# Kernel tuning notes

Hardware: AMD Instinct MI355X
Metric: run time of the kernel (lower is better)

Reference implementation:

```python
import jax, jax.numpy as jnp
import numpy as np

B, S, D, H = 2, 2048, 1024, 16
W = D // H  # head width = 64


def setup_inputs() -> dict:
    key = jax.random.key(0)
    ks = jax.random.split(key, 10)
    std = 1.0 / np.sqrt(D)
    return {
        "x": jax.random.normal(ks[0], (B, S, D), jnp.float32),
        "seg": jax.random.randint(ks[1], (B, S), 0, 2, jnp.int64),
        "Wq": jax.random.normal(ks[2], (D, D), jnp.float32) * std,
        "bq": jnp.zeros((D,), jnp.float32),
        "Wk": jax.random.normal(ks[3], (D, D), jnp.float32) * std,
        "bk": jnp.zeros((D,), jnp.float32),
        "Wv": jax.random.normal(ks[4], (D, D), jnp.float32) * std,
        "bv": jnp.zeros((D,), jnp.float32),
        "Wo": jax.random.normal(ks[5], (D, D), jnp.float32) * std,
        "bo": jnp.zeros((D,), jnp.float32),
    }


def reference(x, seg, Wq, bq, Wk, bk, Wv, bv, Wo, bo):
    # QKV projections: (B,S,D)
    q = x @ Wq + bq
    k = x @ Wk + bk
    v = x @ Wv + bv
    # split heads -> (B,H,S,W)
    def heads(t):
        return t.reshape(B, S, H, W).transpose(0, 2, 1, 3)
    q, k, v = heads(q), heads(k), heads(v)
    scale = 1.0 / np.sqrt(W).astype(np.float32)
    scores = jnp.einsum("bhqw,bhkw->bhqk", q, k) * scale  # (B,H,S,S)
    # causal mask: strictly-upper-triangular entries -> -inf
    causal = jnp.tril(jnp.ones((S, S), dtype=bool))
    scores = jnp.where(causal, scores, -jnp.inf)
    attn = jax.nn.softmax(scores, axis=-1)
    h = jnp.einsum("bhqk,bhkw->bhqw", attn, v)  # (B,H,S,W)
    h = h.transpose(0, 2, 1, 3).reshape(B, S, D)  # merge heads
    return h @ Wo + bo
```

## Files before the change

### kernel.cpp

```cpp
#include <hip/hip_runtime.h>

#define BB 2
#define SS 2048
#define DD 1024
#define HH 16
#define WW 64
#define MM (BB*SS)

typedef float f32x4 __attribute__((ext_vector_type(4)));
typedef short s16x8 __attribute__((ext_vector_type(8)));
typedef short s16x4 __attribute__((ext_vector_type(4)));

__device__ __forceinline__ unsigned short f2bf(float f) {
  return __builtin_bit_cast(unsigned short, (__bf16)f);
}
__device__ __forceinline__ float bf2f(unsigned short u) {
  return (float)__builtin_bit_cast(__bf16, u);
}
__device__ __forceinline__ void dma16(const unsigned short* g, unsigned short* l) {
  __builtin_amdgcn_global_load_lds(
      (const __attribute__((address_space(1))) unsigned int*)g,
      (__attribute__((address_space(3))) unsigned int*)l, 16, 0, 0);
}

__global__ __launch_bounds__(256) void k_prep(const float* __restrict__ x,
                                              unsigned short* __restrict__ xb,
                                              const float* __restrict__ W0,
                                              const float* __restrict__ W1,
                                              const float* __restrict__ W2,
                                              const float* __restrict__ W3,
                                              unsigned short* __restrict__ T0,
                                              unsigned short* __restrict__ T1,
                                              unsigned short* __restrict__ T2,
                                              unsigned short* __restrict__ T3) {
  if (blockIdx.z >= 4) {
    int blk = (blockIdx.z - 4) * 1024 + blockIdx.y * 32 + blockIdx.x;
    int i = (blk * 256 + threadIdx.x) * 4;
    float4 v = *(const float4*)(x + i);
    *(ushort4*)(xb + i) = make_ushort4(f2bf(v.x), f2bf(v.y), f2bf(v.z), f2bf(v.w));
    return;
  }
  const float* Wm = blockIdx.z == 0 ? W0 : blockIdx.z == 1 ? W1 : blockIdx.z == 2 ? W2 : W3;
  unsigned short* Wt = blockIdx.z == 0 ? T0 : blockIdx.z == 1 ? T1 : blockIdx.z == 2 ? T2 : T3;
  __shared__ float tile[32][33];
  int bn = blockIdx.x * 32;
  int bk = blockIdx.y * 32;
  int tx = threadIdx.x & 31;
  int ty = threadIdx.x >> 5;
#pragma unroll
  for (int r = 0; r < 4; ++r)
    tile[ty + r * 8][tx] = Wm[(bk + ty + r * 8) * DD + bn + tx];
  __syncthreads();
#pragma unroll
  for (int r = 0; r < 4; ++r)
    Wt[(bn + ty + r * 8) * DD + bk + tx] = f2bf(tile[tx][ty + r * 8]);
}

__global__ __launch_bounds__(256, 3) void k_gemm_qkv(const unsigned short* __restrict__ A,
                                                     const unsigned short* __restrict__ Wcat,
                                                     const float* __restrict__ bq,
                                                     const float* __restrict__ bk,
                                                     const float* __restrict__ bv,
                                                     unsigned short* __restrict__ Qo,
                                                     unsigned short* __restrict__ Ko,
                                                     unsigned short* __restrict__ Vo) {
  __shared__ __align__(16) unsigned short As[2][128 * 32];
  __shared__ __align__(16) unsigned short Bs[2][128 * 32];
  const int widx = blockIdx.x >> 3;
  const int n0 = (blockIdx.x & 7) * 128;
  const int m0 = blockIdx.y * 128;
  const unsigned short* Bt = Wcat + (size_t)widx * DD * DD;
  const float* bias = widx == 0 ? bq : widx == 1 ? bk : bv;
  unsigned short* outp = widx == 0 ? Qo : widx == 1 ? Ko : Vo;
  const float oscale = widx == 0 ? 0.125f * 1.4426950408889634f : 1.0f;
  const int t = threadIdx.x;
  const int wv = t >> 6, lane = t & 63;
  const int quad = lane >> 4, l16 = lane & 15;
  const int wm = (wv >> 1) * 64, wn = (wv & 1) * 64;
  const unsigned short* srcA[2];
  const unsigned short* srcB[2];
  int dstoff[2];
#pragma unroll
  for (int d = 0; d < 2; ++d) {
    int s = d * 256 + wv * 64 + lane;
    int r = s >> 2, pb = s & 3;
    int lc = ((pb ^ (r & 3)) << 3);
    srcA[d] = A + (size_t)(m0 + r) * DD + lc;
    srcB[d] = Bt + (size_t)(n0 + r) * DD + lc;
    dstoff[d] = (d * 256 + wv * 64) * 8;
  }
  f32x4 acc[4][4] = {};

#pragma unroll
  for (int d = 0; d < 2; ++d) {
    dma16(srcA[d], &As[0][dstoff[d]]);
    dma16(srcB[d], &Bs[0][dstoff[d]]);
  }

  for (int it = 0; it < DD / 32; ++it) {
    asm volatile("s_waitcnt vmcnt(0)" ::: "memory");
    __syncthreads();
    if (it + 1 < DD / 32) {
      const int nb = (it + 1) & 1;
      const int k1 = (it + 1) * 32;
#pragma unroll
      for (int d = 0; d < 2; ++d) {
        dma16(srcA[d] + k1, &As[nb][dstoff[d]]);
        dma16(srcB[d] + k1, &Bs[nb][dstoff[d]]);
      }
    }
    const unsigned short* Asb = As[it & 1];
    const unsigned short* Bsb = Bs[it & 1];
    s16x8 af[4], bfr[4];
#pragma unroll
    for (int mi = 0; mi < 4; ++mi) {
      int ra = wm + mi * 16 + l16;
      af[mi] = *(const s16x8*)(Asb + ra * 32 + ((quad ^ (ra & 3)) << 3));
    }
#pragma unroll
    for (int ni = 0; ni < 4; ++ni) {
      int rb = wn + ni * 16 + l16;
      bfr[ni] = *(const s16x8*)(Bsb + rb * 32 + ((quad ^ (rb & 3)) << 3));
    }
#pragma unroll
    for (int mi = 0; mi < 4; ++mi)
#pragma unroll
      for (int ni = 0; ni < 4; ++ni)
        acc[mi][ni] = __builtin_amdgcn_mfma_f32_16x16x32_bf16(af[mi], bfr[ni], acc[mi][ni], 0, 0, 0);
  }

#pragma unroll
  for (int mi = 0; mi < 4; ++mi) {
#pragma unroll
    for (int ni = 0; ni < 4; ++ni) {
      int col = n0 + wn + ni * 16 + l16;
      float bb = bias[col];
      int h = col >> 6, w = col & 63;
#pragma unroll
      for (int r = 0; r < 4; ++r) {
        int row = m0 + wm + mi * 16 + quad * 4 + r;
        float v = (acc[mi][ni][r] + bb) * oscale;
        int b = row >> 11, s = row & (SS - 1);
        long off;
        if (widx == 2) off = (long)(b * HH + h) * (SS * WW) + (long)w * SS + s;
        else           off = (long)(b * HH + h) * (SS * WW) + (long)s * WW + w;
        outp[off] = f2bf(v);
      }
    }
  }
}

__global__ __launch_bounds__(256, 3) void k_gemm_out(const unsigned short* __restrict__ A,
                                                     const unsigned short* __restrict__ Bt,
                                                     const float* __restrict__ bias,
                                                     float* __restrict__ out_f) {
  __shared__ __align__(16) unsigned short As[2][128 * 32];
  __shared__ __align__(16) unsigned short Bs[2][64 * 32];
  const int m0 = blockIdx.y * 128, n0 = blockIdx.x * 64;
  const int t = threadIdx.x;
  const int wv = t >> 6, lane = t & 63;
  const int quad = lane >> 4, l16 = lane & 15;
  const int wm = (wv >> 1) * 64, wn = (wv & 1) * 32;
  const unsigned short* srcA[2];
  int dstA[2];
#pragma unroll
  for (int d = 0; d < 2; ++d) {
    int s = d * 256 + wv * 64 + lane;
    int r = s >> 2, pb = s & 3;
    int lc = ((pb ^ (r & 3)) << 3);
    srcA[d] = A + (size_t)(m0 + r) * DD + lc;
    dstA[d] = (d * 256 + wv * 64) * 8;
  }
  const int sB = wv * 64 + lane;
  const int rB = sB >> 2, pbB = sB & 3;
  const unsigned short* srcB = Bt + (size_t)(n0 + rB) * DD + ((pbB ^ (rB & 3)) << 3);
  const int dstB = (wv * 64) * 8;
  f32x4 acc[4][2] = {};

#pragma unroll
  for (int d = 0; d < 2; ++d) dma16(srcA[d], &As[0][dstA[d]]);
  dma16(srcB, &Bs[0][dstB]);

  for (int it = 0; it < DD / 32; ++it) {
    asm volatile("s_waitcnt vmcnt(0)" ::: "memory");
    __syncthreads();
    if (it + 1 < DD / 32) {
      const int nb = (it + 1) & 1;
      const int k1 = (it + 1) * 32;
#pragma unroll
      for (int d = 0; d < 2; ++d) dma16(srcA[d] + k1, &As[nb][dstA[d]]);
      dma16(srcB + k1, &Bs[nb][dstB]);
    }
    const unsigned short* Asb = As[it & 1];
    const unsigned short* Bsb = Bs[it & 1];
    s16x8 af[4], bfr[2];
#pragma unroll
    for (int mi = 0; mi < 4; ++mi) {
      int ra = wm + mi * 16 + l16;
      af[mi] = *(const s16x8*)(Asb + ra * 32 + ((quad ^ (ra & 3)) << 3));
    }
#pragma unroll
    for (int ni = 0; ni < 2; ++ni) {
      int rb = wn + ni * 16 + l16;
      bfr[ni] = *(const s16x8*)(Bsb + rb * 32 + ((quad ^ (rb & 3)) << 3));
    }
#pragma unroll
    for (int mi = 0; mi < 4; ++mi)
#pragma unroll
      for (int ni = 0; ni < 2; ++ni)
        acc[mi][ni] = __builtin_amdgcn_mfma_f32_16x16x32_bf16(af[mi], bfr[ni], acc[mi][ni], 0, 0, 0);
  }

#pragma unroll
  for (int mi = 0; mi < 4; ++mi)
#pragma unroll
    for (int ni = 0; ni < 2; ++ni) {
      int col = n0 + wn + ni * 16 + l16;
      float bb = bias[col];
#pragma unroll
      for (int r = 0; r < 4; ++r) {
        int row = m0 + wm + mi * 16 + quad * 4 + r;
        out_f[row * DD + col] = acc[mi][ni][r] + bb;
      }
    }
}

__global__ __launch_bounds__(256, 2) void k_attn_mfma(const unsigned short* __restrict__ Q,
                                                      const unsigned short* __restrict__ K,
                                                      const unsigned short* __restrict__ Vt,
                                                      unsigned short* __restrict__ hm) {
  __shared__ __align__(16) unsigned short Kbuf[2][128 * 64];
  __shared__ __align__(16) unsigned short Vbuf[2][64 * 128];
  const int id = blockIdx.y * 16 + blockIdx.x;
  const int xcd = id & 7;
  const int j = id >> 3;
  const int bh = xcd * 4 + (j & 3);
  const int px = j >> 2;
  const int pairp = px >> 1;
  const int qh = px & 1;
  const int t = threadIdx.x;
  const int wv = t >> 6, lane = t & 63;
  const int quad = lane >> 4, l16 = lane & 15;
  const unsigned short* Qp = Q + (size_t)bh * SS * WW;
  const unsigned short* Kp = K + (size_t)bh * SS * WW;
  const unsigned short* Vp = Vt + (size_t)bh * WW * SS;
  const int b = bh >> 4, h = bh & 15;

  const int rrK = lane >> 3;
  const int kswz = (((lane & 7) ^ rrK) << 3);

  for (int sp = 0; sp < 2; ++sp) {
    const int strip = sp == 0 ? pairp : 15 - pairp;
    const int qs = strip * 128;
    const int qb = qs + qh * 64 + wv * 16;

    s16x8 qf[2];
#pragma unroll
    for (int c = 0; c < 2; ++c)
      qf[c] = *(const s16x8*)(Qp + (qb + l16) * WW + c * 32 + quad * 8);

    f32x4 O[4] = {};
    float l = 0.f;

    const int nkt = strip + 1;

#pragma unroll
    for (int d = 0; d < 4; ++d) {
      const int D = wv * 4 + d;
      dma16(Kp + (size_t)(D * 8 + rrK) * WW + kswz, &Kbuf[0][D * 512]);
      const int vrow = D * 4 + quad;
      dma16(Vp + (size_t)vrow * SS + (((lane & 15) ^ (vrow & 7)) << 3), &Vbuf[0][D * 512]);
    }

    for (int kt = 0; kt < nkt; ++kt) {
      const int kb = kt * 128;
      asm volatile("s_waitcnt vmcnt(0)" ::: "memory");
      __syncthreads();
      if (kt + 1 < nkt) {
        const int nb = (kt + 1) & 1;
        const int kbn = kb + 128;
#pragma unroll
        for (int d = 0; d < 4; ++d) {
          const int D = wv * 4 + d;
          dma16(Kp + (size_t)(kbn + D * 8 + rrK) * WW + kswz, &Kbuf[nb][D * 512]);
          const int vrow = D * 4 + quad;
          dma16(Vp + (size_t)vrow * SS + kbn + (((lane & 15) ^ (vrow & 7)) << 3),
                &Vbuf[nb][D * 512]);
        }
      }
      const unsigned short* Kb_ = Kbuf[kt & 1];
      const unsigned short* Vb_ = Vbuf[kt & 1];

      s16x8 kf[8][2];
#pragma unroll
      for (int mt = 0; mt < 8; ++mt)
#pragma unroll
        for (int c = 0; c < 2; ++c)
          kf[mt][c] = *(const s16x8*)(Kb_ + (mt * 16 + l16) * 64 + (((c * 4 + quad) ^ (l16 & 7)) << 3));

      f32x4 sc[8] = {};
      __builtin_amdgcn_s_setprio(1);
#pragma unroll
      for (int mt = 0; mt < 8; ++mt)
#pragma unroll
        for (int c = 0; c < 2; ++c)
          sc[mt] = __builtin_amdgcn_mfma_f32_16x16x32_bf16(kf[mt][c], qf[c], sc[mt], 0, 0, 0);
      __builtin_amdgcn_s_setprio(0);

      if (kt == nkt - 1) {
#pragma unroll
        for (int mt = 0; mt < 8; ++mt)
#pragma unroll
          for (int r = 0; r < 4; ++r)
            if (kb + mt * 16 + quad * 4 + r > qb + l16)
              sc[mt][r] = -__builtin_inff();
      }

#pragma unroll
      for (int mt = 0; mt < 8; ++mt)
#pragma unroll
        for (int r = 0; r < 4; ++r)
          sc[mt][r] = __builtin_amdgcn_exp2f(sc[mt][r]);

      s16x8 pf[4];
#pragma unroll
      for (int c = 0; c < 4; ++c) {
#pragma unroll
        for (int e = 0; e < 4; ++e) {
          pf[c][e]     = (short)f2bf(sc[2 * c][e]);
          pf[c][4 + e] = (short)f2bf(sc[2 * c + 1][e]);
        }
      }

      float ts[8];
#pragma unroll
      for (int mt = 0; mt < 8; ++mt)
        ts[mt] = (sc[mt][0] + sc[mt][1]) + (sc[mt][2] + sc[mt][3]);
      l += ((ts[0] + ts[1]) + (ts[2] + ts[3])) + ((ts[4] + ts[5]) + (ts[6] + ts[7]));

      const int xr = l16 & 7;
      __builtin_amdgcn_s_setprio(1);
#pragma unroll
      for (int ni = 0; ni < 4; ++ni) {
        const unsigned short* vrp = Vb_ + (ni * 16 + l16) * 128 + ((quad & 1) << 2);
#pragma unroll
        for (int c = 0; c < 4; ++c) {
          const int blo = (4 * c + (quad >> 1)) ^ xr;
          const int bhi = (4 * c + 2 + (quad >> 1)) ^ xr;
          s16x4 vlo = *(const s16x4*)(vrp + (blo << 3));
          s16x4 vhi = *(const s16x4*)(vrp + (bhi << 3));
          s16x8 vfc = __builtin_shufflevector(vlo, vhi, 0, 1, 2, 3, 4, 5, 6, 7);
          O[ni] = __builtin_amdgcn_mfma_f32_16x16x32_bf16(pf[c], vfc, O[ni], 0, 0, 0);
        }
      }
      __builtin_amdgcn_s_setprio(0);
    }

    l += __shfl_xor(l, 16);
    l += __shfl_xor(l, 32);
#pragma unroll
    for (int r = 0; r < 4; ++r) {
      const float linv = 1.f / __shfl(l, quad * 4 + r);
      const int q = qb + quad * 4 + r;
#pragma unroll
      for (int ni = 0; ni < 4; ++ni)
        hm[(size_t)(b * SS + q) * DD + h * WW + ni * 16 + l16] = f2bf(O[ni][r] * linv);
    }
    __syncthreads();
  }
}

extern "C" void kernel_launch(void* const* d_in, const int* in_sizes, int n_in,
                              void* d_out, int out_size, void* d_ws, size_t ws_size,
                              hipStream_t stream) {
  const float* x  = (const float*)d_in[0];
  const float* Wq = (const float*)d_in[2];
  const float* bq = (const float*)d_in[3];
  const float* Wk = (const float*)d_in[4];
  const float* bk = (const float*)d_in[5];
  const float* Wv = (const float*)d_in[6];
  const float* bv = (const float*)d_in[7];
  const float* Wo = (const float*)d_in[8];
  const float* bo = (const float*)d_in[9];
  float* out = (float*)d_out;

  char* ws = (char*)d_ws;
  unsigned short* xb   = (unsigned short*)(ws);
  unsigned short* Wcat = (unsigned short*)(ws + (size_t)( 8 << 20));
  unsigned short* Wtq  = Wcat;
  unsigned short* Wtk  = Wcat + (size_t)DD * DD;
  unsigned short* Wtv  = Wcat + (size_t)2 * DD * DD;
  unsigned short* Wto  = (unsigned short*)(ws + (size_t)(14 << 20));
  unsigned short* Qb   = (unsigned short*)(ws + (size_t)(16 << 20));
  unsigned short* Kb   = (unsigned short*)(ws + (size_t)(24 << 20));
  unsigned short* Vtb  = (unsigned short*)(ws + (size_t)(32 << 20));
  unsigned short* hm   = (unsigned short*)(ws + (size_t)(40 << 20));

  dim3 pg(32, 32, 8);
  k_prep<<<pg, 256, 0, stream>>>(x, xb, Wq, Wk, Wv, Wo, Wtq, Wtk, Wtv, Wto);

  dim3 gq(24, MM / 128);
  k_gemm_qkv<<<gq, 256, 0, stream>>>(xb, Wcat, bq, bk, bv, Qb, Kb, Vtb);

  dim3 ag(16, BB * HH);
  k_attn_mfma<<<ag, 256, 0, stream>>>(Qb, Kb, Vtb, hm);

  dim3 go(DD / 64, MM / 128);
  k_gemm_out<<<go, 256, 0, stream>>>(hm, Wto, bo, out);
}
```

Before: 188.3 us.

## Fuse all four stages into one persistent kernel with grid-wide barriers

Merges the prep/transposition, QKV GEMM, attention and output GEMM kernels into a single persistent 512-block kernel that loops over virtual block indices and separates stages with a software grid barrier built on global atomics. The goal is to remove three kernel launch gaps and their tail drains. In exchange every stage runs with a fixed 512-block grid at 2 blocks per CU, the QKV GEMM loses its previous 3-block occupancy hint, and correctness depends on all 512 blocks being co-resident. The barrier counter and generation live in device globals that persist across calls.

```diff
diff --git a/kernel.cpp b/kernel.cpp
--- a/kernel.cpp
+++ b/kernel.cpp
@@ -14,359 +14,373 @@
 __device__ __forceinline__ unsigned short f2bf(float f) {
   return __builtin_bit_cast(unsigned short, (__bf16)f);
 }
-__device__ __forceinline__ float bf2f(unsigned short u) {
-  return (float)__builtin_bit_cast(__bf16, u);
-}
 __device__ __forceinline__ void dma16(const unsigned short* g, unsigned short* l) {
   __builtin_amdgcn_global_load_lds(
       (const __attribute__((address_space(1))) unsigned int*)g,
       (__attribute__((address_space(3))) unsigned int*)l, 16, 0, 0);
 }
 
-__global__ __launch_bounds__(256) void k_prep(const float* __restrict__ x,
-                                              unsigned short* __restrict__ xb,
-                                              const float* __restrict__ W0,
-                                              const float* __restrict__ W1,
-                                              const float* __restrict__ W2,
-                                              const float* __restrict__ W3,
-                                              unsigned short* __restrict__ T0,
-                                              unsigned short* __restrict__ T1,
-                                              unsigned short* __restrict__ T2,
-                                              unsigned short* __restrict__ T3) {
-  if (blockIdx.z >= 4) {
-    int blk = (blockIdx.z - 4) * 1024 + blockIdx.y * 32 + blockIdx.x;
-    int i = (blk * 256 + threadIdx.x) * 4;
-    float4 v = *(const float4*)(x + i);
-    *(ushort4*)(xb + i) = make_ushort4(f2bf(v.x), f2bf(v.y), f2bf(v.z), f2bf(v.w));
-    return;
+__device__ unsigned g_count = 0;
+__device__ unsigned g_gen = 0;
+
+__device__ __forceinline__ void grid_sync() {
+  __syncthreads();
+  if (threadIdx.x == 0) {
+    __threadfence();
+    unsigned gen = __hip_atomic_load(&g_gen, __ATOMIC_RELAXED, __HIP_MEMORY_SCOPE_AGENT);
+    unsigned n = __hip_atomic_fetch_add(&g_count, 1u, __ATOMIC_ACQ_REL, __HIP_MEMORY_SCOPE_AGENT);
+    if (n + 1u == 512u) {
+      __hip_atomic_store(&g_count, 0u, __ATOMIC_RELAXED, __HIP_MEMORY_SCOPE_AGENT);
+      __hip_atomic_store(&g_gen, gen + 1u, __ATOMIC_RELEASE, __HIP_MEMORY_SCOPE_AGENT);
+    } else {
+      while (__hip_atomic_load(&g_gen, __ATOMIC_ACQUIRE, __HIP_MEMORY_SCOPE_AGENT) == gen)
+        __builtin_amdgcn_s_sleep(16);
+    }
+    __threadfence();
   }
-  const float* Wm = blockIdx.z == 0 ? W0 : blockIdx.z == 1 ? W1 : blockIdx.z == 2 ? W2 : W3;
-  unsigned short* Wt = blockIdx.z == 0 ? T0 : blockIdx.z == 1 ? T1 : blockIdx.z == 2 ? T2 : T3;
-  __shared__ float tile[32][33];
-  int bn = blockIdx.x * 32;
-  int bk = blockIdx.y * 32;
-  int tx = threadIdx.x & 31;
-  int ty = threadIdx.x >> 5;
-#pragma unroll
-  for (int r = 0; r < 4; ++r)
-    tile[ty + r * 8][tx] = Wm[(bk + ty + r * 8) * DD + bn + tx];
   __syncthreads();
-#pragma unroll
-  for (int r = 0; r < 4; ++r)
-    Wt[(bn + ty + r * 8) * DD + bk + tx] = f2bf(tile[tx][ty + r * 8]);
 }
 
-__global__ __launch_bounds__(256, 3) void k_gemm_qkv(const unsigned short* __restrict__ A,
-                                                     const unsigned short* __restrict__ Wcat,
-                                                     const float* __restrict__ bq,
-                                                     const float* __restrict__ bk,
-                                                     const float* __restrict__ bv,
-                                                     unsigned short* __restrict__ Qo,
-                                                     unsigned short* __restrict__ Ko,
-                                                     unsigned short* __restrict__ Vo) {
-  __shared__ __align__(16) unsigned short As[2][128 * 32];
-  __shared__ __align__(16) unsigned short Bs[2][128 * 32];
-  const int widx = blockIdx.x >> 3;
-  const int n0 = (blockIdx.x & 7) * 128;
-  const int m0 = blockIdx.y * 128;
-  const unsigned short* Bt = Wcat + (size_t)widx * DD * DD;
-  const float* bias = widx == 0 ? bq : widx == 1 ? bk : bv;
-  unsigned short* outp = widx == 0 ? Qo : widx == 1 ? Ko : Vo;
-  const float oscale = widx == 0 ? 0.125f * 1.4426950408889634f : 1.0f;
+__global__ __launch_bounds__(256, 2) void k_fused(
+    const float* __restrict__ x,
+    const float* __restrict__ Wq, const float* __restrict__ bq,
+    const float* __restrict__ Wk, const float* __restrict__ bk,
+    const float* __restrict__ Wv, const float* __restrict__ bv,
+    const float* __restrict__ Wo, const float* __restrict__ bo,
+    unsigned short* __restrict__ xb, unsigned short* __restrict__ Wcat,
+    unsigned short* __restrict__ Wto, unsigned short* __restrict__ Qg,
+    unsigned short* __restrict__ Kg, unsigned short* __restrict__ Vg,
+    unsigned short* __restrict__ hm, float* __restrict__ out) {
+  __shared__ __align__(16) unsigned char smem[65536];
+  const int blk = blockIdx.x;
   const int t = threadIdx.x;
-  const int wv = t >> 6, lane = t & 63;
+  const int wvi = t >> 6, lane = t & 63;
   const int quad = lane >> 4, l16 = lane & 15;
-  const int wm = (wv >> 1) * 64, wn = (wv & 1) * 64;
-  const unsigned short* srcA[2];
-  const unsigned short* srcB[2];
-  int dstoff[2];
-#pragma unroll
-  for (int d = 0; d < 2; ++d) {
-    int s = d * 256 + wv * 64 + lane;
-    int r = s >> 2, pb = s & 3;
-    int lc = ((pb ^ (r & 3)) << 3);
-    srcA[d] = A + (size_t)(m0 + r) * DD + lc;
-    srcB[d] = Bt + (size_t)(n0 + r) * DD + lc;
-    dstoff[d] = (d * 256 + wv * 64) * 8;
+
+  {
+    float(*tile)[33] = (float(*)[33])smem;
+    const int tx = t & 31, ty = t >> 5;
+    for (int i = 0; i < 16; ++i) {
+      const int v = blk * 16 + i;
+      const int vz = v >> 10;
+      if (vz >= 4) {
+        const int idx = ((v - 4096) * 256 + t) * 4;
+        float4 vv = *(const float4*)(x + idx);
+        *(ushort4*)(xb + idx) = make_ushort4(f2bf(vv.x), f2bf(vv.y), f2bf(vv.z), f2bf(vv.w));
+      } else {
+        const int vy = (v >> 5) & 31, vx = v & 31;
+        const float* Wm = vz == 0 ? Wq : vz == 1 ? Wk : vz == 2 ? Wv : Wo;
+        unsigned short* Wt = vz == 3 ? Wto : Wcat + (size_t)vz * DD * DD;
+        const int bn = vx * 32, bk_ = vy * 32;
+#pragma unroll
+        for (int r = 0; r < 4; ++r)
+          tile[ty + r * 8][tx] = Wm[(size_t)(bk_ + ty + r * 8) * DD + bn + tx];
+        __syncthreads();
+#pragma unroll
+        for (int r = 0; r < 4; ++r)
+          Wt[(size_t)(bn + ty + r * 8) * DD + bk_ + tx] = f2bf(tile[tx][ty + r * 8]);
+        __syncthreads();
+      }
+    }
   }
-  f32x4 acc[4][4] = {};
-
-#pragma unroll
-  for (int d = 0; d < 2; ++d) {
-    dma16(srcA[d], &As[0][dstoff[d]]);
-    dma16(srcB[d], &Bs[0][dstoff[d]]);
+  grid_sync();
+
+  {
+    unsigned short* As = (unsigned short*)smem;
+    unsigned short* Bs = (unsigned short*)(smem + 16384);
+    for (int rep = 0; rep < 2; ++rep) {
+      const int v = rep == 0 ? blk : 512 + blk;
+      if (v >= 768) break;
+      const int gx = v % 24, gy = v / 24;
+      const int widx = gx >> 3;
+      const int n0 = (gx & 7) * 128;
+      const int m0 = gy * 128;
+      const unsigned short* Bt = Wcat + (size_t)widx * DD * DD;
+      const float* bias = widx == 0 ? bq : widx == 1 ? bk : bv;
+      unsigned short* outp = widx == 0 ? Qg : widx == 1 ? Kg : Vg;
+      const float oscale = widx == 0 ? 0.125f * 1.4426950408889634f : 1.0f;
+      const int wm = (wvi >> 1) * 64, wn = (wvi & 1) * 64;
+      const unsigned short* srcA[2];
+      const unsigned short* srcB[2];
+      int dstoff[2];
+#pragma unroll
+      for (int d = 0; d < 2; ++d) {
+        int s = d * 256 + wvi * 64 + lane;
+        int r = s >> 2, pb = s & 3;
+        int lc = ((pb ^ (r & 3)) << 3);
+        srcA[d] = xb + (size_t)(m0 + r) * DD + lc;
+        srcB[d] = Bt + (size_t)(n0 + r) * DD + lc;
+        dstoff[d] = (d * 256 + wvi * 64) * 8;
+      }
+      f32x4 acc[4][4] = {};
+
+#pragma unroll
+      for (int d = 0; d < 2; ++d) {
+        dma16(srcA[d], As + dstoff[d]);
+        dma16(srcB[d], Bs + dstoff[d]);
+      }
+
+      for (int it = 0; it < DD / 32; ++it) {
+        asm volatile("s_waitcnt vmcnt(0)" ::: "memory");
+        __syncthreads();
+        if (it + 1 < DD / 32) {
+          const int nb = (it + 1) & 1;
+          const int k1 = (it + 1) * 32;
+#pragma unroll
+          for (int d = 0; d < 2; ++d) {
+            dma16(srcA[d] + k1, As + nb * 4096 + dstoff[d]);
+            dma16(srcB[d] + k1, Bs + nb * 4096 + dstoff[d]);
+          }
+        }
+        const unsigned short* Asb = As + (it & 1) * 4096;
+        const unsigned short* Bsb = Bs + (it & 1) * 4096;
+        s16x8 af[4], bfr[4];
+#pragma unroll
+        for (int mi = 0; mi < 4; ++mi) {
+          int ra = wm + mi * 16 + l16;
+          af[mi] = *(const s16x8*)(Asb + ra * 32 + ((quad ^ (ra & 3)) << 3));
+        }
+#pragma unroll
+        for (int ni = 0; ni < 4; ++ni) {
+          int rb = wn + ni * 16 + l16;
+          bfr[ni] = *(const s16x8*)(Bsb + rb * 32 + ((quad ^ (rb & 3)) << 3));
+        }
+#pragma unroll
+        for (int mi = 0; mi < 4; ++mi)
+#pragma unroll
+          for (int ni = 0; ni < 4; ++ni)
+            acc[mi][ni] = __builtin_amdgcn_mfma_f32_16x16x32_bf16(af[mi], bfr[ni], acc[mi][ni], 0, 0, 0);
+      }
+
+#pragma unroll
+      for (int mi = 0; mi < 4; ++mi) {
+#pragma unroll
+        for (int ni = 0; ni < 4; ++ni) {
+          int col = n0 + wn + ni * 16 + l16;
+          float bb = bias[col];
+          int h = col >> 6, w = col & 63;
+#pragma unroll
+          for (int r = 0; r < 4; ++r) {
+            int row = m0 + wm + mi * 16 + quad * 4 + r;
+            float vv = (acc[mi][ni][r] + bb) * oscale;
+            int b = row >> 11, s = row & (SS - 1);
+            long off;
+            if (widx == 2) off = (long)(b * HH + h) * (SS * WW) + (long)w * SS + s;
+            else           off = (long)(b * HH + h) * (SS * WW) + (long)s * WW + w;
+            outp[off] = f2bf(vv);
+          }
+        }
+      }
+      __syncthreads();
+    }
   }
-
-  for (int it = 0; it < DD / 32; ++it) {
-    asm volatile("s_waitcnt vmcnt(0)" ::: "memory");
-    __syncthreads();
-    if (it + 1 < DD / 32) {
-      const int nb = (it + 1) & 1;
-      const int k1 = (it + 1) * 32;
-#pragma unroll
-      for (int d = 0; d < 2; ++d) {
-        dma16(srcA[d] + k1, &As[nb][dstoff[d]]);
-        dma16(srcB[d] + k1, &Bs[nb][dstoff[d]]);
-      }
-    }
-    const unsigned short* Asb = As[it & 1];
-    const unsigned short* Bsb = Bs[it & 1];
-    s16x8 af[4], bfr[4];
-#pragma unroll
-    for (int mi = 0; mi < 4; ++mi) {
-      int ra = wm + mi * 16 + l16;
-      af[mi] = *(const s16x8*)(Asb + ra * 32 + ((quad ^ (ra & 3)) << 3));
-    }
-#pragma unroll
-    for (int ni = 0; ni < 4; ++ni) {
-      int rb = wn + ni * 16 + l16;
-      bfr[ni] = *(const s16x8*)(Bsb + rb * 32 + ((quad ^ (rb & 3)) << 3));
-    }
-#pragma unroll
-    for (int mi = 0; mi < 4; ++mi)
-#pragma unroll
-      for (int ni = 0; ni < 4; ++ni)
-        acc[mi][ni] = __builtin_amdgcn_mfma_f32_16x16x32_bf16(af[mi], bfr[ni], acc[mi][ni], 0, 0, 0);
+  grid_sync();
+
+  {
+    unsigned short* Ksh = (unsigned short*)smem;
+    unsigned short* Vsh = (unsigned short*)(smem + 32768);
+    const int id = blk;
+    const int xcd = id & 7;
+    const int j = id >> 3;
+    const int bh = xcd * 4 + (j & 3);
+    const int px = j >> 2;
+    const int pairp = px >> 1;
+    const int qh = px & 1;
+    const unsigned short* Qp = Qg + (size_t)bh * SS * WW;
+    const unsigned short* Kp = Kg + (size_t)bh * SS * WW;
+    const unsigned short* Vp = Vg + (size_t)bh * WW * SS;
+    const int b = bh >> 4, h = bh & 15;
+    const int rrK = lane >> 3;
+    const int kswz = (((lane & 7) ^ rrK) << 3);
+
+    for (int sp = 0; sp < 2; ++sp) {
+      const int strip = sp == 0 ? pairp : 15 - pairp;
+      const int qs = strip * 128;
+      const int qb = qs + qh * 64 + wvi * 16;
+
+      s16x8 qf[2];
+#pragma unroll
+      for (int c = 0; c < 2; ++c)
+        qf[c] = *(const s16x8*)(Qp + (qb + l16) * WW + c * 32 + quad * 8);
+
+      f32x4 O[4] = {};
+      float l = 0.f;
+      const int nkt = strip + 1;
+
+#pragma unroll
+      for (int d = 0; d < 4; ++d) {
+        const int D = wvi * 4 + d;
+        dma16(Kp + (size_t)(D * 8 + rrK) * WW + kswz, Ksh + D * 512);
+        const int vrow = D * 4 + quad;
+        dma16(Vp + (size_t)vrow * SS + (((lane & 15) ^ (vrow & 7)) << 3), Vsh + D * 512);
+      }
+
+      for (int kt = 0; kt < nkt; ++kt) {
+        const int kb = kt * 128;
+        asm volatile("s_waitcnt vmcnt(0)" ::: "memory");
+        __syncthreads();
+        if (kt + 1 < nkt) {
+          const int nb = (kt + 1) & 1;
+          const int kbn = kb + 128;
+#pragma unroll
+          for (int d = 0; d < 4; ++d) {
+            const int D = wvi * 4 + d;
+            dma16(Kp + (size_t)(kbn + D * 8 + rrK) * WW + kswz, Ksh + nb * 8192 + D * 512);
+            const int vrow = D * 4 + quad;
+            dma16(Vp + (size_t)vrow * SS + kbn + (((lane & 15) ^ (vrow & 7)) << 3),
+                  Vsh + nb * 8192 + D * 512);
+          }
+        }
+        const unsigned short* Kb_ = Ksh + (kt & 1) * 8192;
+        const unsigned short* Vb_ = Vsh + (kt & 1) * 8192;
+
+        s16x8 kf[8][2];
+#pragma unroll
+        for (int mt = 0; mt < 8; ++mt)
+#pragma unroll
+          for (int c = 0; c < 2; ++c)
+            kf[mt][c] = *(const s16x8*)(Kb_ + (mt * 16 + l16) * 64 + (((c * 4 + quad) ^ (l16 & 7)) << 3));
+
+        f32x4 sc[8] = {};
+        __builtin_amdgcn_s_setprio(1);
+#pragma unroll
+        for (int mt = 0; mt < 8; ++mt)
+#pragma unroll
+          for (int c = 0; c < 2; ++c)
+            sc[mt] = __builtin_amdgcn_mfma_f32_16x16x32_bf16(kf[mt][c], qf[c], sc[mt], 0, 0, 0);
+        __builtin_amdgcn_s_setprio(0);
+
+        if (kt == nkt - 1) {
+#pragma unroll
+          for (int mt = 0; mt < 8; ++mt)
+#pragma unroll
+            for (int r = 0; r < 4; ++r)
+              if (kb + mt * 16 + quad * 4 + r > qb + l16)
+                sc[mt][r] = -__builtin_inff();
+        }
+
+#pragma unroll
+        for (int mt = 0; mt < 8; ++mt)
+#pragma unroll
+          for (int r = 0; r < 4; ++r)
+            sc[mt][r] = __builtin_amdgcn_exp2f(sc[mt][r]);
+
+        s16x8 pf[4];
+#pragma unroll
+        for (int c = 0; c < 4; ++c) {
+#pragma unroll
+          for (int e = 0; e < 4; ++e) {
+            pf[c][e]     = (short)f2bf(sc[2 * c][e]);
+            pf[c][4 + e] = (short)f2bf(sc[2 * c + 1][e]);
+          }
+        }
+
+        float ts[8];
+#pragma unroll
+        for (int mt = 0; mt < 8; ++mt)
+          ts[mt] = (sc[mt][0] + sc[mt][1]) + (sc[mt][2] + sc[mt][3]);
+        l += ((ts[0] + ts[1]) + (ts[2] + ts[3])) + ((ts[4] + ts[5]) + (ts[6] + ts[7]));
+
+        const int xr = l16 & 7;
+        __builtin_amdgcn_s_setprio(1);
+#pragma unroll
+        for (int ni = 0; ni < 4; ++ni) {
+          const unsigned short* vrp = Vb_ + (ni * 16 + l16) * 128 + ((quad & 1) << 2);
+#pragma unroll
+          for (int c = 0; c < 4; ++c) {
+            const int blo = (4 * c + (quad >> 1)) ^ xr;
+            const int bhi = (4 * c + 2 + (quad >> 1)) ^ xr;
+            s16x4 vlo = *(const s16x4*)(vrp + (blo << 3));
+            s16x4 vhi = *(const s16x4*)(vrp + (bhi << 3));
+            s16x8 vfc = __builtin_shufflevector(vlo, vhi, 0, 1, 2, 3, 4, 5, 6, 7);
+            O[ni] = __builtin_amdgcn_mfma_f32_16x16x32_bf16(pf[c], vfc, O[ni], 0, 0, 0);
+          }
+        }
+        __builtin_amdgcn_s_setprio(0);
+      }
+
+      l += __shfl_xor(l, 16);
+      l += __shfl_xor(l, 32);
+#pragma unroll
+      for (int r = 0; r < 4; ++r) {
+        const float linv = 1.f / __shfl(l, quad * 4 + r);
+        const int q = qb + quad * 4 + r;
+#pragma unroll
+        for (int ni = 0; ni < 4; ++ni)
+          hm[(size_t)(b * SS + q) * DD + h * WW + ni * 16 + l16] = f2bf(O[ni][r] * linv);
+      }
+      __syncthreads();
+    }
   }
-
-#pragma unroll
-  for (int mi = 0; mi < 4; ++mi) {
-#pragma unroll
-    for (int ni = 0; ni < 4; ++ni) {
-      int col = n0 + wn + ni * 16 + l16;
-      float bb = bias[col];
-      int h = col >> 6, w = col & 63;
-#pragma unroll
-      for (int r = 0; r < 4; ++r) {
-        int row = m0 + wm + mi * 16 + quad * 4 + r;
-        float v = (acc[mi][ni][r] + bb) * oscale;
-        int b = row >> 11, s = row & (SS - 1);
-        long off;
-        if (widx == 2) off = (long)(b * HH + h) * (SS * WW) + (long)w * SS + s;
-        else           off = (long)(b * HH + h) * (SS * WW) + (long)s * WW + w;
-        outp[off] = f2bf(v);
-      }
-    }
-  }
-}
-
-__global__ __launch_bounds__(256, 3) void k_gemm_out(const unsigned short* __restrict__ A,
-                                                     const unsigned short* __restrict__ Bt,
-                                                     const float* __restrict__ bias,
-                                                     float* __restrict__ out_f) {
-  __shared__ __align__(16) unsigned short As[2][128 * 32];
-  __shared__ __align__(16) unsigned short Bs[2][64 * 32];
-  const int m0 = blockIdx.y * 128, n0 = blockIdx.x * 64;
-  const int t = threadIdx.x;
-  const int wv = t >> 6, lane = t & 63;
-  const int quad = lane >> 4, l16 = lane & 15;
-  const int wm = (wv >> 1) * 64, wn = (wv & 1) * 32;
-  const unsigned short* srcA[2];
-  int dstA[2];
-#pragma unroll
-  for (int d = 0; d < 2; ++d) {
-    int s = d * 256 + wv * 64 + lane;
-    int r = s >> 2, pb = s & 3;
-    int lc = ((pb ^ (r & 3)) << 3);
-    srcA[d] = A + (size_t)(m0 + r) * DD + lc;
-    dstA[d] = (d * 256 + wv * 64) * 8;
-  }
-  const int sB = wv * 64 + lane;
-  const int rB = sB >> 2, pbB = sB & 3;
-  const unsigned short* srcB = Bt + (size_t)(n0 + rB) * DD + ((pbB ^ (rB & 3)) << 3);
-  const int dstB = (wv * 64) * 8;
-  f32x4 acc[4][2] = {};
-
-#pragma unroll
-  for (int d = 0; d < 2; ++d) dma16(srcA[d], &As[0][dstA[d]]);
-  dma16(srcB, &Bs[0][dstB]);
-
-  for (int it = 0; it < DD / 32; ++it) {
-    asm volatile("s_waitcnt vmcnt(0)" ::: "memory");
-    __syncthreads();
-    if (it + 1 < DD / 32) {
-      const int nb = (it + 1) & 1;
-      const int k1 = (it + 1) * 32;
-#pragma unroll
-      for (int d = 0; d < 2; ++d) dma16(srcA[d] + k1, &As[nb][dstA[d]]);
-      dma16(srcB + k1, &Bs[nb][dstB]);
-    }
-    const unsigned short* Asb = As[it & 1];
-    const unsigned short* Bsb = Bs[it & 1];
-    s16x8 af[4], bfr[2];
-#pragma unroll
-    for (int mi = 0; mi < 4; ++mi) {
-      int ra = wm + mi * 16 + l16;
-      af[mi] = *(const s16x8*)(Asb + ra * 32 + ((quad ^ (ra & 3)) << 3));
-    }
-#pragma unroll
-    for (int ni = 0; ni < 2; ++ni) {
-      int rb = wn + ni * 16 + l16;
-      bfr[ni] = *(const s16x8*)(Bsb + rb * 32 + ((quad ^ (rb & 3)) << 3));
-    }
-#pragma unroll
-    for (int mi = 0; mi < 4; ++mi)
-#pragma unroll
-      for (int ni = 0; ni < 2; ++ni)
-        acc[mi][ni] = __builtin_amdgcn_mfma_f32_16x16x32_bf16(af[mi], bfr[ni], acc[mi][ni], 0, 0, 0);
-  }
-
-#pragma unroll
-  for (int mi = 0; mi < 4; ++mi)
-#pragma unroll
-    for (int ni = 0; ni < 2; ++ni) {
-      int col = n0 + wn + ni * 16 + l16;
-      float bb = bias[col];
-#pragma unroll
-      for (int r = 0; r < 4; ++r) {
-        int row = m0 + wm + mi * 16 + quad * 4 + r;
-        out_f[row * DD + col] = acc[mi][ni][r] + bb;
-      }
-    }
-}
-
-__global__ __launch_bounds__(256, 2) void k_attn_mfma(const unsigned short* __restrict__ Q,
-                                                      const unsigned short* __restrict__ K,
-                                                      const unsigned short* __restrict__ Vt,
-                                                      unsigned short* __restrict__ hm) {
-  __shared__ __align__(16) unsigned short Kbuf[2][128 * 64];
-  __shared__ __align__(16) unsigned short Vbuf[2][64 * 128];
-  const int id = blockIdx.y * 16 + blockIdx.x;
-  const int xcd = id & 7;
-  const int j = id >> 3;
-  const int bh = xcd * 4 + (j & 3);
-  const int px = j >> 2;
-  const int pairp = px >> 1;
-  const int qh = px & 1;
-  const int t = threadIdx.x;
-  const int wv = t >> 6, lane = t & 63;
-  const int quad = lane >> 4, l16 = lane & 15;
-  const unsigned short* Qp = Q + (size_t)bh * SS * WW;
-  const unsigned short* Kp = K + (size_t)bh * SS * WW;
-  const unsigned short* Vp = Vt + (size_t)bh * WW * SS;
-  const int b = bh >> 4, h = bh & 15;
-
-  const int rrK = lane >> 3;
-  const int kswz = (((lane & 7) ^ rrK) << 3);
-
-  for (int sp = 0; sp < 2; ++sp) {
-    const int strip = sp == 0 ? pairp : 15 - pairp;
-    const int qs = strip * 128;
-    const int qb = qs + qh * 64 + wv * 16;
-
-    s16x8 qf[2];
-#pragma unroll
-    for (int c = 0; c < 2; ++c)
-      qf[c] = *(const s16x8*)(Qp + (qb + l16) * WW + c * 32 + quad * 8);
-
-    f32x4 O[4] = {};
-    float l = 0.f;
-
-    const int nkt = strip + 1;
-
-#pragma unroll
-    for (int d = 0; d < 4; ++d) {
-      const int D = wv * 4 + d;
-      dma16(Kp + (size_t)(D * 8 + rrK) * WW + kswz, &Kbuf[0][D * 512]);
-      const int vrow = D * 4 + quad;
-      dma16(Vp + (size_t)vrow * SS + (((lane & 15) ^ (vrow & 7)) << 3), &Vbuf[0][D * 512]);
-    }
-
-    for (int kt = 0; kt < nkt; ++kt) {
-      const int kb = kt * 128;
+  grid_sync();
+
+  {
+    unsigned short* As = (unsigned short*)smem;
+    unsigned short* Bs = (unsigned short*)(smem + 16384);
+    const int m0 = (blk >> 4) * 128, n0 = (blk & 15) * 64;
+    const int wm = (wvi >> 1) * 64, wn = (wvi & 1) * 32;
+    const unsigned short* srcA[2];
+    int dstA[2];
+#pragma unroll
+    for (int d = 0; d < 2; ++d) {
+      int s = d * 256 + wvi * 64 + lane;
+      int r = s >> 2, pb = s & 3;
+      int lc = ((pb ^ (r & 3)) << 3);
+      srcA[d] = hm + (size_t)(m0 + r) * DD + lc;
+      dstA[d] = (d * 256 + wvi * 64) * 8;
+    }
+    const int sB = wvi * 64 + lane;
+    const int rB = sB >> 2, pbB = sB & 3;
+    const unsigned short* srcB = Wto + (size_t)(n0 + rB) * DD + ((pbB ^ (rB & 3)) << 3);
+    const int dstB = (wvi * 64) * 8;
+    f32x4 acc[4][2] = {};
+
+#pragma unroll
+    for (int d = 0; d < 2; ++d) dma16(srcA[d], As + dstA[d]);
+    dma16(srcB, Bs + dstB);
+
+    for (int it = 0; it < DD / 32; ++it) {
       asm volatile("s_waitcnt vmcnt(0)" ::: "memory");
       __syncthreads();
-      if (kt + 1 < nkt) {
-        const int nb = (kt + 1) & 1;
-        const int kbn = kb + 128;
-#pragma unroll
-        for (int d = 0; d < 4; ++d) {
-          const int D = wv * 4 + d;
-          dma16(Kp + (size_t)(kbn + D * 8 + rrK) * WW + kswz, &Kbuf[nb][D * 512]);
-          const int vrow = D * 4 + quad;
-          dma16(Vp + (size_t)vrow * SS + kbn + (((lane & 15) ^ (vrow & 7)) << 3),
-                &Vbuf[nb][D * 512]);
-        }
-      }
-      const unsigned short* Kb_ = Kbuf[kt & 1];
-      const unsigned short* Vb_ = Vbuf[kt & 1];
-
-      s16x8 kf[8][2];
-#pragma unroll
-      for (int mt = 0; mt < 8; ++mt)
-#pragma unroll
-        for (int c = 0; c < 2; ++c)
-          kf[mt][c] = *(const s16x8*)(Kb_ + (mt * 16 + l16) * 64 + (((c * 4 + quad) ^ (l16 & 7)) << 3));
-
-      f32x4 sc[8] = {};
-      __builtin_amdgcn_s_setprio(1);
-#pragma unroll
-      for (int mt = 0; mt < 8; ++mt)
-#pragma unroll
-        for (int c = 0; c < 2; ++c)
-          sc[mt] = __builtin_amdgcn_mfma_f32_16x16x32_bf16(kf[mt][c], qf[c], sc[mt], 0, 0, 0);
-      __builtin_amdgcn_s_setprio(0);
-
-      if (kt == nkt - 1) {
-#pragma unroll
-        for (int mt = 0; mt < 8; ++mt)
-#pragma unroll
-          for (int r = 0; r < 4; ++r)
-            if (kb + mt * 16 + quad * 4 + r > qb + l16)
-              sc[mt][r] = -__builtin_inff();
-      }
-
-#pragma unroll
-      for (int mt = 0; mt < 8; ++mt)
-#pragma unroll
-        for (int r = 0; r < 4; ++r)
-          sc[mt][r] = __builtin_amdgcn_exp2f(sc[mt][r]);
-
-      s16x8 pf[4];
-#pragma unroll
-      for (int c = 0; c < 4; ++c) {
-#pragma unroll
-        for (int e = 0; e < 4; ++e) {
-          pf[c][e]     = (short)f2bf(sc[2 * c][e]);
-          pf[c][4 + e] = (short)f2bf(sc[2 * c + 1][e]);
-        }
-      }
-
-      float ts[8];
-#pragma unroll
-      for (int mt = 0; mt < 8; ++mt)
-        ts[mt] = (sc[mt][0] + sc[mt][1]) + (sc[mt][2] + sc[mt][3]);
-      l += ((ts[0] + ts[1]) + (ts[2] + ts[3])) + ((ts[4] + ts[5]) + (ts[6] + ts[7]));
-
-      const int xr = l16 & 7;
-      __builtin_amdgcn_s_setprio(1);
-#pragma unroll
-      for (int ni = 0; ni < 4; ++ni) {
-        const unsigned short* vrp = Vb_ + (ni * 16 + l16) * 128 + ((quad & 1) << 2);
-#pragma unroll
-        for (int c = 0; c < 4; ++c) {
-          const int blo = (4 * c + (quad >> 1)) ^ xr;
-          const int bhi = (4 * c + 2 + (quad >> 1)) ^ xr;
-          s16x4 vlo = *(const s16x4*)(vrp + (blo << 3));
-          s16x4 vhi = *(const s16x4*)(vrp + (bhi << 3));
-          s16x8 vfc = __builtin_shufflevector(vlo, vhi, 0, 1, 2, 3, 4, 5, 6, 7);
-          O[ni] = __builtin_amdgcn_mfma_f32_16x16x32_bf16(pf[c], vfc, O[ni], 0, 0, 0);
-        }
-      }
-      __builtin_amdgcn_s_setprio(0);
-    }
-
-    l += __shfl_xor(l, 16);
-    l += __shfl_xor(l, 32);
-#pragma unroll
-    for (int r = 0; r < 4; ++r) {
-      const float linv = 1.f / __shfl(l, quad * 4 + r);
-      const int q = qb + quad * 4 + r;
-#pragma unroll
-      for (int ni = 0; ni < 4; ++ni)
-        hm[(size_t)(b * SS + q) * DD + h * WW + ni * 16 + l16] = f2bf(O[ni][r] * linv);
-    }
-    __syncthreads();
+      if (it + 1 < DD / 32) {
+        const int nb = (it + 1) & 1;
+        const int k1 = (it + 1) * 32;
+#pragma unroll
+        for (int d = 0; d < 2; ++d) dma16(srcA[d] + k1, As + nb * 4096 + dstA[d]);
+        dma16(srcB + k1, Bs + nb * 2048 + dstB);
+      }
+      const unsigned short* Asb = As + (it & 1) * 4096;
+      const unsigned short* Bsb = Bs + (it & 1) * 2048;
+      s16x8 af[4], bfr[2];
+#pragma unroll
+      for (int mi = 0; mi < 4; ++mi) {
+        int ra = wm + mi * 16 + l16;
+        af[mi] = *(const s16x8*)(Asb + ra * 32 + ((quad ^ (ra & 3)) << 3));
+      }
+#pragma unroll
+      for (int ni = 0; ni < 2; ++ni) {
+        int rb = wn + ni * 16 + l16;
+        bfr[ni] = *(const s16x8*)(Bsb + rb * 32 + ((quad ^ (rb & 3)) << 3));
+      }
+#pragma unroll
+      for (int mi = 0; mi < 4; ++mi)
+#pragma unroll
+        for (int ni = 0; ni < 2; ++ni)
+          acc[mi][ni] = __builtin_amdgcn_mfma_f32_16x16x32_bf16(af[mi], bfr[ni], acc[mi][ni], 0, 0, 0);
+    }
+
+#pragma unroll
+    for (int mi = 0; mi < 4; ++mi)
+#pragma unroll
+      for (int ni = 0; ni < 2; ++ni) {
+        int col = n0 + wn + ni * 16 + l16;
+        float bb = bo[col];
+#pragma unroll
+        for (int r = 0; r < 4; ++r) {
+          int row = m0 + wm + mi * 16 + quad * 4 + r;
+          out[(size_t)row * DD + col] = acc[mi][ni][r] + bb;
+        }
+      }
   }
 }
 
@@ -387,24 +401,12 @@
   char* ws = (char*)d_ws;
   unsigned short* xb   = (unsigned short*)(ws);
   unsigned short* Wcat = (unsigned short*)(ws + (size_t)( 8 << 20));
-  unsigned short* Wtq  = Wcat;
-  unsigned short* Wtk  = Wcat + (size_t)DD * DD;
-  unsigned short* Wtv  = Wcat + (size_t)2 * DD * DD;
   unsigned short* Wto  = (unsigned short*)(ws + (size_t)(14 << 20));
   unsigned short* Qb   = (unsigned short*)(ws + (size_t)(16 << 20));
   unsigned short* Kb   = (unsigned short*)(ws + (size_t)(24 << 20));
   unsigned short* Vtb  = (unsigned short*)(ws + (size_t)(32 << 20));
   unsigned short* hm   = (unsigned short*)(ws + (size_t)(40 << 20));
 
-  dim3 pg(32, 32, 8);
-  k_prep<<<pg, 256, 0, stream>>>(x, xb, Wq, Wk, Wv, Wo, Wtq, Wtk, Wtv, Wto);
-
-  dim3 gq(24, MM / 128);
-  k_gemm_qkv<<<gq, 256, 0, stream>>>(xb, Wcat, bq, bk, bv, Qb, Kb, Vtb);
-
-  dim3 ag(16, BB * HH);
-  k_attn_mfma<<<ag, 256, 0, stream>>>(Qb, Kb, Vtb, hm);
-
-  dim3 go(DD / 64, MM / 128);
-  k_gemm_out<<<go, 256, 0, stream>>>(hm, Wto, bo, out);
+  k_fused<<<dim3(512), dim3(256), 0, stream>>>(x, Wq, bq, Wk, bk, Wv, bv, Wo, bo,
+                                               xb, Wcat, Wto, Qb, Kb, Vtb, hm, out);
 }
```

Result: slower. 524.2 us (+178.3%).
